# Kernel optimization log

Hardware: AMD Instinct MI355X
Metric: run time of the kernel (lower is better)

## Reference

```python
import jax, jax.numpy as jnp
import numpy as np

EPS = 1e-6
NUM_SEMANTICS = 8
HIDDEN = 768
BATCH = 4096


def _gram_schmidt_single(vectors, fallback):
    """Sequential (classical, per-torch-code) Gram-Schmidt on (S, D) vectors.
    fallback: (S, D) random vectors used when a residual norm falls below EPS.
    """
    S = vectors.shape[0]
    qs = []
    for i in range(S):
        v = vectors[i]
        for j in range(i):
            qj = qs[j]
            denom = jnp.dot(qj, qj)
            safe_denom = jnp.where(denom > 0, denom, 1.0)
            proj = jnp.dot(v, qj) / safe_denom
            # torch: only subtract if ||q_j|| > eps
            v = jnp.where(jnp.sqrt(denom) > EPS, v - proj * qj, v)
        norm = jnp.linalg.norm(v)
        safe_norm = jnp.where(norm > 0, norm, 1.0)
        fb = fallback[i]
        fb = fb / jnp.linalg.norm(fb)
        q = jnp.where(norm > EPS, v / safe_norm, fb)
        qs.append(q)
    return jnp.stack(qs, axis=0)


def setup_inputs() -> dict:
    key = jax.random.key(0)
    semantic_reprs = jax.random.normal(key, (BATCH, NUM_SEMANTICS, HIDDEN), dtype=jnp.float32)
    return {"semantic_reprs": semantic_reprs}


def reference(semantic_reprs):
    B, S, D = semantic_reprs.shape
    # fixed fallback random vectors (stand-in for torch.randn_like in the degenerate branch)
    fallback = jax.random.normal(jax.random.key(42), (B, S, D), dtype=semantic_reprs.dtype)
    return jax.vmap(_gram_schmidt_single)(semantic_reprs, fallback)
```

## Files before the change

### kernel.cpp

```cpp
#include <hip/hip_runtime.h>


#define S_VECS 8
#define D_DIM 768
#define EPL 12
#define F4_PER_VEC 192

typedef float f32x4 __attribute__((ext_vector_type(4)));

__device__ __forceinline__ float wave_reduce_sum(float x) {
#pragma unroll
    for (int off = 32; off >= 1; off >>= 1)
        x += __shfl_xor(x, off, 64);
    return x;
}

__global__ __launch_bounds__(256, 4)
void gram_schmidt_kernel(const float* __restrict__ in, float* __restrict__ out, int B) {
    const int wave = threadIdx.x >> 6;
    const int lane = threadIdx.x & 63;
    const int b = blockIdx.x * 4 + wave;
    if (b >= B) return;

    float v[S_VECS][EPL];
    const f32x4* src = reinterpret_cast<const f32x4*>(in) + (size_t)b * (S_VECS * F4_PER_VEC);
#pragma unroll
    for (int s = 0; s < S_VECS; ++s) {
#pragma unroll
        for (int k = 0; k < 3; ++k) {
            f32x4 f = src[s * F4_PER_VEC + k * 64 + lane];
            v[s][k * 4 + 0] = f.x;
            v[s][k * 4 + 1] = f.y;
            v[s][k * 4 + 2] = f.z;
            v[s][k * 4 + 3] = f.w;
        }
    }

    float inv_n[S_VECS];

#pragma unroll
    for (int i = 1; i < S_VECS; ++i) {
        float d[S_VECS];
#pragma unroll
        for (int j = 0; j < S_VECS; ++j) {
            if (j < i) {
                float acc = 0.f;
#pragma unroll
                for (int e = 0; e < EPL; ++e) acc += v[i][e] * v[j][e];
                d[j] = acc;
            }
        }
        float self = 0.f;
#pragma unroll
        for (int e = 0; e < EPL; ++e) self += v[i - 1][e] * v[i - 1][e];

#pragma unroll
        for (int j = 0; j < S_VECS; ++j) {
            if (j < i) d[j] = wave_reduce_sum(d[j]);
        }
        self = wave_reduce_sum(self);
        inv_n[i - 1] = 1.0f / self;

#pragma unroll
        for (int j = 0; j < S_VECS; ++j) {
            if (j < i) {
                const float proj = d[j] * inv_n[j];
#pragma unroll
                for (int e = 0; e < EPL; ++e) v[i][e] -= proj * v[j][e];
            }
        }
    }
    {
        float self = 0.f;
#pragma unroll
        for (int e = 0; e < EPL; ++e) self += v[S_VECS - 1][e] * v[S_VECS - 1][e];
        self = wave_reduce_sum(self);
        inv_n[S_VECS - 1] = 1.0f / self;
    }

    f32x4* dst = reinterpret_cast<f32x4*>(out) + (size_t)b * (S_VECS * F4_PER_VEC);
#pragma unroll
    for (int s = 0; s < S_VECS; ++s) {
        const float inv_norm = sqrtf(inv_n[s]);
#pragma unroll
        for (int k = 0; k < 3; ++k) {
            f32x4 f;
            f.x = v[s][k * 4 + 0] * inv_norm;
            f.y = v[s][k * 4 + 1] * inv_norm;
            f.z = v[s][k * 4 + 2] * inv_norm;
            f.w = v[s][k * 4 + 3] * inv_norm;
            __builtin_nontemporal_store(f, &dst[s * F4_PER_VEC + k * 64 + lane]);
        }
    }
}

extern "C" void kernel_launch(void* const* d_in, const int* in_sizes, int n_in,
                              void* d_out, int out_size, void* d_ws, size_t ws_size,
                              hipStream_t stream) {
    const float* in = (const float*)d_in[0];
    float* out = (float*)d_out;
    const int B = in_sizes[0] / (S_VECS * D_DIM);
    const int blocks = (B + 3) / 4;
    gram_schmidt_kernel<<<blocks, 256, 0, stream>>>(in, out, B);
}
```

Measured before the change: 42.70 us.

## Split each batch item across three waves with LDS cross-wave reductions

Each batch element is now handled by a 192-thread block of three waves instead of a single wave. Every thread holds only 4 floats per vector instead of 12, which cuts register pressure and raises the number of threads working on the problem. Each wave's partial dot products are combined through double-buffered shared memory and a block barrier at every Gram-Schmidt step. The cost is seven or eight __syncthreads per block plus LDS traffic, which adds latency to a dependency chain that is already serial.

```diff
diff --git a/kernel.cpp b/kernel.cpp
--- a/kernel.cpp
+++ b/kernel.cpp
@@ -3,8 +3,7 @@
 
 #define S_VECS 8
 #define D_DIM 768
-#define EPL 12
-#define F4_PER_VEC 192
+#define CHUNKS 192
 
 typedef float f32x4 __attribute__((ext_vector_type(4)));
 
@@ -15,50 +14,64 @@
     return x;
 }
 
-__global__ __launch_bounds__(256, 4)
-void gram_schmidt_kernel(const float* __restrict__ in, float* __restrict__ out, int B) {
+__global__ __launch_bounds__(192)
+void gram_schmidt_kernel(const float* __restrict__ in, float* __restrict__ out) {
     const int wave = threadIdx.x >> 6;
     const int lane = threadIdx.x & 63;
-    const int b = blockIdx.x * 4 + wave;
-    if (b >= B) return;
+    const int b = blockIdx.x;
+    const int chunk = wave * 64 + lane;
 
-    float v[S_VECS][EPL];
-    const f32x4* src = reinterpret_cast<const f32x4*>(in) + (size_t)b * (S_VECS * F4_PER_VEC);
+    __shared__ float red[2][S_VECS][3];
+
+    const int w1 = (wave == 2) ? 0 : wave + 1;
+    const int w2 = (wave == 0) ? 2 : wave - 1;
+
+    float v[S_VECS][4];
+    const f32x4* src = reinterpret_cast<const f32x4*>(in) + (size_t)b * (S_VECS * CHUNKS);
 #pragma unroll
     for (int s = 0; s < S_VECS; ++s) {
-#pragma unroll
-        for (int k = 0; k < 3; ++k) {
-            f32x4 f = src[s * F4_PER_VEC + k * 64 + lane];
-            v[s][k * 4 + 0] = f.x;
-            v[s][k * 4 + 1] = f.y;
-            v[s][k * 4 + 2] = f.z;
-            v[s][k * 4 + 3] = f.w;
-        }
+        f32x4 f = src[s * CHUNKS + chunk];
+        v[s][0] = f.x; v[s][1] = f.y; v[s][2] = f.z; v[s][3] = f.w;
     }
 
     float inv_n[S_VECS];
 
 #pragma unroll
     for (int i = 1; i < S_VECS; ++i) {
+        const int p = i & 1;
         float d[S_VECS];
 #pragma unroll
         for (int j = 0; j < S_VECS; ++j) {
             if (j < i) {
                 float acc = 0.f;
 #pragma unroll
-                for (int e = 0; e < EPL; ++e) acc += v[i][e] * v[j][e];
+                for (int e = 0; e < 4; ++e) acc += v[i][e] * v[j][e];
                 d[j] = acc;
             }
         }
         float self = 0.f;
 #pragma unroll
-        for (int e = 0; e < EPL; ++e) self += v[i - 1][e] * v[i - 1][e];
+        for (int e = 0; e < 4; ++e) self += v[i - 1][e] * v[i - 1][e];
 
 #pragma unroll
         for (int j = 0; j < S_VECS; ++j) {
             if (j < i) d[j] = wave_reduce_sum(d[j]);
         }
         self = wave_reduce_sum(self);
+
+        if (lane == 0) {
+#pragma unroll
+            for (int j = 0; j < S_VECS; ++j) {
+                if (j < i) red[p][j][wave] = d[j];
+            }
+            red[p][i][wave] = self;
+        }
+        __syncthreads();
+#pragma unroll
+        for (int j = 0; j < S_VECS; ++j) {
+            if (j < i) d[j] += red[p][j][w1] + red[p][j][w2];
+        }
+        self += red[p][i][w1] + red[p][i][w2];
         inv_n[i - 1] = 1.0f / self;
 
 #pragma unroll
@@ -66,31 +79,32 @@
             if (j < i) {
                 const float proj = d[j] * inv_n[j];
 #pragma unroll
-                for (int e = 0; e < EPL; ++e) v[i][e] -= proj * v[j][e];
+                for (int e = 0; e < 4; ++e) v[i][e] -= proj * v[j][e];
             }
         }
     }
+
     {
         float self = 0.f;
 #pragma unroll
-        for (int e = 0; e < EPL; ++e) self += v[S_VECS - 1][e] * v[S_VECS - 1][e];
+        for (int e = 0; e < 4; ++e) self += v[S_VECS - 1][e] * v[S_VECS - 1][e];
         self = wave_reduce_sum(self);
+        if (lane == 0) red[0][0][wave] = self;
+        __syncthreads();
+        self += red[0][0][w1] + red[0][0][w2];
         inv_n[S_VECS - 1] = 1.0f / self;
     }
 
-    f32x4* dst = reinterpret_cast<f32x4*>(out) + (size_t)b * (S_VECS * F4_PER_VEC);
+    f32x4* dst = reinterpret_cast<f32x4*>(out) + (size_t)b * (S_VECS * CHUNKS);
 #pragma unroll
     for (int s = 0; s < S_VECS; ++s) {
         const float inv_norm = sqrtf(inv_n[s]);
-#pragma unroll
-        for (int k = 0; k < 3; ++k) {
-            f32x4 f;
-            f.x = v[s][k * 4 + 0] * inv_norm;
-            f.y = v[s][k * 4 + 1] * inv_norm;
-            f.z = v[s][k * 4 + 2] * inv_norm;
-            f.w = v[s][k * 4 + 3] * inv_norm;
-            __builtin_nontemporal_store(f, &dst[s * F4_PER_VEC + k * 64 + lane]);
-        }
+        f32x4 f;
+        f.x = v[s][0] * inv_norm;
+        f.y = v[s][1] * inv_norm;
+        f.z = v[s][2] * inv_norm;
+        f.w = v[s][3] * inv_norm;
+        __builtin_nontemporal_store(f, &dst[s * CHUNKS + chunk]);
     }
 }
 
@@ -100,6 +114,5 @@
     const float* in = (const float*)d_in[0];
     float* out = (float*)d_out;
     const int B = in_sizes[0] / (S_VECS * D_DIM);
-    const int blocks = (B + 3) / 4;
-    gram_schmidt_kernel<<<blocks, 256, 0, stream>>>(in, out, B);
+    gram_schmidt_kernel<<<B, 192, 0, stream>>>(in, out);
 }
```

After: 42.50 us, median of 2. No clear change (-0.5%).
